# Performance work log

Measured on AMD Instinct MI355X. Metric: run time of the kernel, lower is better.

The kernel has to match this reference:

```python
import jax, jax.numpy as jnp
import numpy as np

B, T, DIM = 4, 2048, 512
HEADS, HD = 8, 64
RANK = 256
WIN = 256
EPS = 1e-6
ROPE_BASE = 10000.0


def _rope_tables(seq_len, head_dim):
    pos = jnp.arange(seq_len, dtype=jnp.float32)                      # [T]
    inv_freq = 1.0 / (ROPE_BASE ** (jnp.arange(0, head_dim, 2, dtype=jnp.float32) / head_dim))  # [HD/2]
    ang = pos[:, None] * inv_freq[None, :]                            # [T, HD/2]
    cos = jnp.concatenate([jnp.cos(ang), jnp.cos(ang)], axis=-1)      # [T, HD]
    sin = jnp.concatenate([jnp.sin(ang), jnp.sin(ang)], axis=-1)
    return cos, sin


def _rotate_half(x):
    x1, x2 = jnp.split(x, 2, axis=-1)
    return jnp.concatenate([-x2, x1], axis=-1)


def _apply_rope(q, k):
    # q, k: [B, H, T, HD]
    cos, sin = _rope_tables(q.shape[2], q.shape[3])
    cos = cos[None, None]; sin = sin[None, None]
    q = q * cos + _rotate_half(q) * sin
    k = k * cos + _rotate_half(k) * sin
    return q, k


def _rmsnorm(x, w):
    x32 = x.astype(jnp.float32)
    n = x32 * jax.lax.rsqrt(jnp.mean(x32 * x32, axis=-1, keepdims=True) + EPS)
    return n.astype(x.dtype) * w


def setup_inputs() -> dict:
    key = jax.random.key(0)
    ks = jax.random.split(key, 6)
    s = 0.02
    return {
        "x": jax.random.normal(ks[0], (B, T, DIM), dtype=jnp.float32),
        "Wq": jax.random.normal(ks[1], (DIM, DIM), dtype=jnp.float32) * s,
        "Wkv_down": jax.random.normal(ks[2], (RANK, DIM), dtype=jnp.float32) * s,
        "kv_norm_w": jnp.ones((RANK,), dtype=jnp.float32),
        "Wkv_up": jax.random.normal(ks[3], (2 * DIM, RANK), dtype=jnp.float32) * s,
        "Wout": jax.random.normal(ks[4], (DIM, DIM), dtype=jnp.float32) * s,
    }


def reference(x, Wq, Wkv_down, kv_norm_w, Wkv_up, Wout):
    # q projection -> [B, H, T, HD]
    q = jnp.einsum('btd,ed->bte', x, Wq).reshape(B, T, HEADS, HD).transpose(0, 2, 1, 3)
    # latent KV: down-proj -> RMSNorm -> up-proj
    c_kv = jnp.einsum('btd,rd->btr', x, Wkv_down)          # [B, T, RANK]
    c_kv = _rmsnorm(c_kv, kv_norm_w)
    kv = jnp.einsum('btr,er->bte', c_kv, Wkv_up)            # [B, T, 2*DIM]
    kv = kv.reshape(B, T, 2, HEADS, HD).transpose(2, 0, 3, 1, 4)
    k, v = kv[0], kv[1]                                     # [B, H, T, HD]
    q, k = _apply_rope(q, k)
    rows = jnp.arange(T)[:, None]
    cols = jnp.arange(T)[None, :]
    mask = jnp.abs(cols - rows) <= WIN                      # [T, T]
    scale = HD ** -0.5
    scores = jnp.einsum('bhtd,bhsd->bhts', q, k) * scale    # [B, H, T, T]
    scores = jnp.where(mask[None, None], scores, jnp.float32(-jnp.inf))
    attn = jax.nn.softmax(scores, axis=-1)
    out = jnp.einsum('bhts,bhsd->bhtd', attn, v)            # [B, H, T, HD]
    out = out.transpose(0, 2, 1, 3).reshape(B, T, DIM)
    return jnp.einsum('btd,ed->bte', out, Wout)
```

## Files before the change

kernel.cpp:

```cpp
#include <hip/hip_runtime.h>
#include <math.h>

#define BB 4
#define TT 2048
#define DIMM 512
#define HEADS 8
#define HDIM 64
#define RANKK 256
#define WINN 256

static constexpr int BT = BB * TT;
#define SC2 0.1803368801111244f

typedef short bf8_t __attribute__((ext_vector_type(8)));
typedef float f32x4 __attribute__((ext_vector_type(4)));

__device__ __forceinline__ unsigned short f2bf(float f) {
    unsigned u = __float_as_uint(f);
    u += 0x7fffu + ((u >> 16) & 1u);
    return (unsigned short)(u >> 16);
}
__device__ __forceinline__ unsigned f2bf2(float a, float b) {
    unsigned r;
    asm("v_cvt_pk_bf16_f32 %0, %1, %2" : "=v"(r) : "v"(a), "v"(b));
    return r;
}

typedef __attribute__((address_space(1))) void gvoid_t;
typedef __attribute__((address_space(3))) void lvoid_t;
__device__ __forceinline__ void gload16(const void* g, void* l) {
    __builtin_amdgcn_global_load_lds((gvoid_t*)g, (lvoid_t*)l, 16, 0, 0);
}
#define WAIT_VM0_BARRIER() do { \
    asm volatile("s_waitcnt vmcnt(0)" ::: "memory"); \
    __builtin_amdgcn_s_barrier(); \
    __builtin_amdgcn_sched_barrier(0); \
} while (0)

__device__ __forceinline__ void cvt4(const float* __restrict__ s,
                                     unsigned short* __restrict__ d, int i) {
    float4 v = *reinterpret_cast<const float4*>(s + i);
    uint2 st = make_uint2(f2bf2(v.x, v.y), f2bf2(v.z, v.w));
    *reinterpret_cast<uint2*>(d + i) = st;
}

__global__ __launch_bounds__(256) void prep_kernel(
    const float* __restrict__ x, const float* __restrict__ Wq,
    const float* __restrict__ Wkd, const float* __restrict__ Wku,
    const float* __restrict__ wn, const float* __restrict__ Wout,
    unsigned short* __restrict__ xb, unsigned short* __restrict__ wcomb,
    unsigned short* __restrict__ wkub, unsigned short* __restrict__ woutb,
    float* __restrict__ cosT, float* __restrict__ sinT) {
    int bid = blockIdx.x;
    if (bid < 4096) {
        cvt4(x, xb, (bid * 256 + threadIdx.x) * 4);
    } else if (bid < 4352) {
        cvt4(Wq, wcomb, ((bid - 4096) * 256 + threadIdx.x) * 4);
    } else if (bid < 4480) {
        cvt4(Wkd, wcomb + DIMM * DIMM, ((bid - 4352) * 256 + threadIdx.x) * 4);
    } else if (bid < 4736) {
        int i = ((bid - 4480) * 256 + threadIdx.x) * 4;
        float4 v = *reinterpret_cast<const float4*>(Wku + i);
        float4 s = *reinterpret_cast<const float4*>(wn + (i & 255));
        uint2 st = make_uint2(f2bf2(v.x * s.x, v.y * s.y), f2bf2(v.z * s.z, v.w * s.w));
        *reinterpret_cast<uint2*>(wkub + i) = st;
    } else if (bid < 4992) {
        cvt4(Wout, woutb, ((bid - 4736) * 256 + threadIdx.x) * 4);
    } else {
        int idx = (bid - 4992) * 256 + threadIdx.x;
        int t = idx >> 5, f = idx & 31;
        double freq = pow(10000.0, -(double)f / 32.0);
        double ang = (double)t * freq;
        cosT[idx] = (float)cos(ang);
        sinT[idx] = (float)sin(ang);
    }
}

template<int MODE, int BM>
__global__ __launch_bounds__(BM * 4) void gemm_bf(const unsigned short* __restrict__ A,
                                                  const unsigned short* __restrict__ W,
                                                  float* __restrict__ Cf,
                                                  unsigned short* __restrict__ O1,
                                                  unsigned short* __restrict__ O2,
                                                  const float* __restrict__ cosT,
                                                  const float* __restrict__ sinT,
                                                  float* __restrict__ ssum,
                                                  int K, int N) {
    __shared__ __align__(16) unsigned short As[2][BM * 64];
    __shared__ __align__(16) unsigned short Ws[2][128 * 64];
    const int tid = threadIdx.x;
    const int lane = tid & 63, w = tid >> 6;
    const int lr = lane & 15, hi = lane >> 4;
    const int m0 = blockIdx.x * BM, n0 = blockIdx.y * 128;
    const int wr = (w >> 1) * 32, wc = (w & 1) * 64;

    f32x4 acc[2][4];
#pragma unroll
    for (int i = 0; i < 2; ++i)
#pragma unroll
        for (int j = 0; j < 4; ++j) acc[i][j] = 0.0f;

    const int NT = K >> 6;
    auto stage = [&](int t, int b) {
        const int kt = t * 64;
#pragma unroll
        for (int c = tid; c < BM * 8; c += BM * 4) {
            int row = c >> 3, sc = ((c & 7) ^ (row & 7)) << 3;
            gload16(A + (size_t)(m0 + row) * K + kt + sc, &As[b][c * 8]);
        }
#pragma unroll
        for (int c = tid; c < 1024; c += BM * 4) {
            int row = c >> 3, sc = ((c & 7) ^ (row & 7)) << 3;
            gload16(W + (size_t)(n0 + row) * K + kt + sc, &Ws[b][c * 8]);
        }
    };

    stage(0, 0);
    WAIT_VM0_BARRIER();
    for (int t = 0; t < NT; ++t) {
        const int cur = t & 1;
        if (t + 1 < NT) stage(t + 1, cur ^ 1);
        bf8_t af[2][2], bw[4][2];
#pragma unroll
        for (int i = 0; i < 2; ++i) {
            int row = wr + i * 16 + lr;
#pragma unroll
            for (int kk = 0; kk < 2; ++kk)
                af[i][kk] = *reinterpret_cast<const bf8_t*>(
                    &As[cur][row * 64 + (((kk * 4 + hi) ^ (row & 7)) << 3)]);
        }
#pragma unroll
        for (int j = 0; j < 4; ++j) {
            int row = wc + j * 16 + lr;
#pragma unroll
            for (int kk = 0; kk < 2; ++kk)
                bw[j][kk] = *reinterpret_cast<const bf8_t*>(
                    &Ws[cur][row * 64 + (((kk * 4 + hi) ^ (row & 7)) << 3)]);
        }
#pragma unroll
        for (int kk = 0; kk < 2; ++kk)
#pragma unroll
            for (int i = 0; i < 2; ++i)
#pragma unroll
                for (int j = 0; j < 4; ++j)
                    acc[i][j] = __builtin_amdgcn_mfma_f32_16x16x32_bf16(af[i][kk], bw[j][kk], acc[i][j], 0, 0, 0);
        if (t + 1 < NT) WAIT_VM0_BARRIER();
    }

    if constexpr (MODE == 0) {
#pragma unroll
        for (int i = 0; i < 2; ++i)
#pragma unroll
            for (int j = 0; j < 4; ++j)
#pragma unroll
                for (int r = 0; r < 4; ++r)
                    Cf[(size_t)(m0 + wr + i * 16 + 4 * hi + r) * N + n0 + wc + j * 16 + lr] = acc[i][j][r];
    } else if (n0 < 512) {
        int h = (n0 + wc) >> 6;
#pragma unroll
        for (int i = 0; i < 2; ++i) {
            int tb = m0 + wr + i * 16 + 4 * hi;
            float4 rv4 = make_float4(1.f, 1.f, 1.f, 1.f);
            if constexpr (MODE == 2) {
                float4 sa = *reinterpret_cast<const float4*>(ssum + tb);
                float4 sb = *reinterpret_cast<const float4*>(ssum + 8192 + tb);
                float4 sc = *reinterpret_cast<const float4*>(ssum + 16384 + tb);
                float4 sd = *reinterpret_cast<const float4*>(ssum + 24576 + tb);
                rv4.x = rsqrtf((sa.x + sb.x + sc.x + sd.x) * (1.0f / RANKK) + 1e-6f);
                rv4.y = rsqrtf((sa.y + sb.y + sc.y + sd.y) * (1.0f / RANKK) + 1e-6f);
                rv4.z = rsqrtf((sa.z + sb.z + sc.z + sd.z) * (1.0f / RANKK) + 1e-6f);
                rv4.w = rsqrtf((sa.w + sb.w + sc.w + sd.w) * (1.0f / RANKK) + 1e-6f);
            }
#pragma unroll
            for (int j = 0; j < 2; ++j)
#pragma unroll
                for (int r = 0; r < 4; ++r) {
                    int t = tb + r;
                    int b = t >> 11, tt = t & 2047;
                    int ff = j * 16 + lr;
                    float rv = (&rv4.x)[r];
                    float x1 = acc[i][j][r] * rv, x2 = acc[i][j + 2][r] * rv;
                    float cc = cosT[tt * 32 + ff], ss = sinT[tt * 32 + ff];
                    unsigned u = f2bf2(x1 * cc - x2 * ss, x2 * cc + x1 * ss);
                    unsigned short* dp = O1 + ((size_t)((b * 8 + h) * 2048 + tt)) * 64;
                    dp[ff]      = (unsigned short)u;
                    dp[ff + 32] = (unsigned short)(u >> 16);
                }
        }
    } else if constexpr (MODE == 1) {
        int cb = n0 - 512 + wc;
        int part = ((n0 - 512) >> 7) * 2 + (w & 1);
#pragma unroll
        for (int i = 0; i < 2; ++i) {
            int tb = m0 + wr + i * 16 + 4 * hi;
#pragma unroll
            for (int r = 0; r < 4; ++r) {
                float ps = acc[i][0][r] * acc[i][0][r] + acc[i][1][r] * acc[i][1][r]
                         + acc[i][2][r] * acc[i][2][r] + acc[i][3][r] * acc[i][3][r];
                ps += __shfl_xor(ps, 1);
                ps += __shfl_xor(ps, 2);
                ps += __shfl_xor(ps, 4);
                ps += __shfl_xor(ps, 8);
                if (lr == 0) ssum[part * 8192 + tb + r] = ps;
            }
#pragma unroll
            for (int j = 0; j < 4; ++j) {
                unsigned a01 = f2bf2(acc[i][j][0], acc[i][j][1]);
                unsigned a23 = f2bf2(acc[i][j][2], acc[i][j][3]);
                unsigned short* dp = O2 + (size_t)tb * 256 + cb + j * 16 + lr;
                dp[0]   = (unsigned short)a01;
                dp[256] = (unsigned short)(a01 >> 16);
                dp[512] = (unsigned short)a23;
                dp[768] = (unsigned short)(a23 >> 16);
            }
        }
    } else {
        int cb = n0 + wc - 512;
        int h = cb >> 6;
#pragma unroll
        for (int i = 0; i < 2; ++i) {
            int tb = m0 + wr + i * 16 + 4 * hi;
            int b = tb >> 11, tt = tb & 2047;
            float4 sa = *reinterpret_cast<const float4*>(ssum + tb);
            float4 sb = *reinterpret_cast<const float4*>(ssum + 8192 + tb);
            float4 sc = *reinterpret_cast<const float4*>(ssum + 16384 + tb);
            float4 sd = *reinterpret_cast<const float4*>(ssum + 24576 + tb);
            float4 rv4;
            rv4.x = rsqrtf((sa.x + sb.x + sc.x + sd.x) * (1.0f / RANKK) + 1e-6f);
            rv4.y = rsqrtf((sa.y + sb.y + sc.y + sd.y) * (1.0f / RANKK) + 1e-6f);
            rv4.z = rsqrtf((sa.z + sb.z + sc.z + sd.z) * (1.0f / RANKK) + 1e-6f);
            rv4.w = rsqrtf((sa.w + sb.w + sc.w + sd.w) * (1.0f / RANKK) + 1e-6f);
#pragma unroll
            for (int j = 0; j < 4; ++j) {
                int hd = j * 16 + lr;
                uint2 st = make_uint2(f2bf2(acc[i][j][0] * rv4.x, acc[i][j][1] * rv4.y),
                                      f2bf2(acc[i][j][2] * rv4.z, acc[i][j][3] * rv4.w));
                *reinterpret_cast<uint2*>(O2 + (((size_t)(b * 8 + h) * 64 + hd) * 2048 + tt)) = st;
            }
        }
    }
}

__global__ __launch_bounds__(512) void attn_mfma(const unsigned short* __restrict__ qbf,
                                                 const unsigned short* __restrict__ kbf,
                                                 const unsigned short* __restrict__ vT,
                                                 unsigned short* __restrict__ aob) {
    __shared__ __align__(16) unsigned short Kl[2][64 * 64];
    __shared__ __align__(16) unsigned short Vl[2][64 * 64];
    __shared__ unsigned short Pl[128][72];
    const int tid = threadIdx.x;
    const int lane = tid & 63, w = tid >> 6;
    const int lr = lane & 15, hi = lane >> 4;

    const int fid = blockIdx.x;
    const int swz = (fid & 7) * 64 + (fid >> 3);
    const int t0 = (swz & 15) * 128;
    const int bh = swz >> 4;

    const unsigned short* qp = qbf + ((size_t)bh * TT + t0 + w * 16 + lr) * HDIM;
    bf8_t qa[2];
    qa[0] = *reinterpret_cast<const bf8_t*>(qp + hi * 8);
    qa[1] = *reinterpret_cast<const bf8_t*>(qp + 32 + hi * 8);

    f32x4 oc[4];
#pragma unroll
    for (int f = 0; f < 4; ++f) oc[f] = 0.0f;
    float lp[4] = {0.f, 0.f, 0.f, 0.f};

    const int smin = max(0, t0 - WINN);
    const int smax = min(TT, t0 + 128 + WINN);
    const int NT = (smax - smin) >> 6;

    const int st_row = tid >> 3;
    const int st_c = tid & 7;
    const int st_cs = (st_c ^ (st_row & 7)) << 3;

    auto stage = [&](int t, int b) {
        const int s0 = smin + t * 64;
        gload16(kbf + ((size_t)bh * TT + s0 + st_row) * HDIM + st_cs, &Kl[b][tid * 8]);
        gload16(vT + ((size_t)bh * 64 + st_row) * TT + s0 + st_cs, &Vl[b][tid * 8]);
    };

    stage(0, 0);
    WAIT_VM0_BARRIER();
    for (int t = 0; t < NT; ++t) {
        const int cur = t & 1;
        if (t + 1 < NT) stage(t + 1, cur ^ 1);
        const int s0 = smin + t * 64;

        f32x4 sacc[4];
#pragma unroll
        for (int f = 0; f < 4; ++f) sacc[f] = 0.0f;
        __builtin_amdgcn_s_setprio(1);
#pragma unroll
        for (int ks = 0; ks < 2; ++ks)
#pragma unroll
            for (int f = 0; f < 4; ++f) {
                int row = f * 16 + lr;
                bf8_t kb = *reinterpret_cast<const bf8_t*>(
                    &Kl[cur][row * 64 + (((ks * 4 + hi) ^ (row & 7)) << 3)]);
                sacc[f] = __builtin_amdgcn_mfma_f32_16x16x32_bf16(qa[ks], kb, sacc[f], 0, 0, 0);
            }
        __builtin_amdgcn_s_setprio(0);

        const int off_w = s0 - t0 - w * 16;
        const bool edge = (off_w + 63 > WINN) || (off_w - 15 < -WINN);
#pragma unroll
        for (int f = 0; f < 4; ++f) {
            float p[4];
#pragma unroll
            for (int r = 0; r < 4; ++r) {
                float v;
                if (edge) {
                    int d = off_w + f * 16 + lr - 4 * hi - r;
                    v = (d <= WINN && d >= -WINN) ? exp2f(sacc[f][r] * SC2) : 0.f;
                } else {
                    v = exp2f(sacc[f][r] * SC2);
                }
                p[r] = v;
                lp[r] += v;
            }
            unsigned a01 = f2bf2(p[0], p[1]);
            unsigned a23 = f2bf2(p[2], p[3]);
            unsigned short* bp = &Pl[w * 16 + 4 * hi][f * 16 + lr];
            bp[0]   = (unsigned short)a01;
            bp[72]  = (unsigned short)(a01 >> 16);
            bp[144] = (unsigned short)a23;
            bp[216] = (unsigned short)(a23 >> 16);
        }

        __builtin_amdgcn_s_setprio(1);
#pragma unroll
        for (int ks = 0; ks < 2; ++ks) {
            bf8_t pa = *reinterpret_cast<const bf8_t*>(&Pl[w * 16 + lr][ks * 32 + hi * 8]);
#pragma unroll
            for (int f = 0; f < 4; ++f) {
                int row = f * 16 + lr;
                bf8_t vb = *reinterpret_cast<const bf8_t*>(
                    &Vl[cur][row * 64 + (((ks * 4 + hi) ^ (row & 7)) << 3)]);
                oc[f] = __builtin_amdgcn_mfma_f32_16x16x32_bf16(pa, vb, oc[f], 0, 0, 0);
            }
        }
        __builtin_amdgcn_s_setprio(0);
        if (t + 1 < NT) WAIT_VM0_BARRIER();
    }

#pragma unroll
    for (int r = 0; r < 4; ++r) {
        lp[r] += __shfl_xor(lp[r], 1);
        lp[r] += __shfl_xor(lp[r], 2);
        lp[r] += __shfl_xor(lp[r], 4);
        lp[r] += __shfl_xor(lp[r], 8);
    }

    int b = bh >> 3, h = bh & 7;
#pragma unroll
    for (int r = 0; r < 4; ++r) {
        float inv = 1.0f / lp[r];
        int t = t0 + w * 16 + 4 * hi + r;
        unsigned short* op = aob + ((size_t)b * TT + t) * DIMM + h * HDIM;
        unsigned u0 = f2bf2(oc[0][r] * inv, oc[1][r] * inv);
        unsigned u1 = f2bf2(oc[2][r] * inv, oc[3][r] * inv);
        op[lr]      = (unsigned short)u0;
        op[16 + lr] = (unsigned short)(u0 >> 16);
        op[32 + lr] = (unsigned short)u1;
        op[48 + lr] = (unsigned short)(u1 >> 16);
    }
}

extern "C" void kernel_launch(void* const* d_in, const int* in_sizes, int n_in,
                              void* d_out, int out_size, void* d_ws, size_t ws_size,
                              hipStream_t stream) {
    const float* x     = (const float*)d_in[0];
    const float* Wq    = (const float*)d_in[1];
    const float* Wkd   = (const float*)d_in[2];
    const float* wnorm = (const float*)d_in[3];
    const float* Wku   = (const float*)d_in[4];
    const float* Wout  = (const float*)d_in[5];
    float* out = (float*)d_out;
    char* ws = (char*)d_ws;

    unsigned short* xb    = (unsigned short*)(ws + 0);
    unsigned short* qb    = (unsigned short*)(ws + 8388608);
    unsigned short* kb    = (unsigned short*)(ws + 16777216);
    unsigned short* vTb   = (unsigned short*)(ws + 25165824);
    unsigned short* ckvb0 = (unsigned short*)(ws + 33554432);
    unsigned short* aob   = (unsigned short*)(ws + 37748736);
    unsigned short* wcomb = (unsigned short*)(ws + 46137344);
    unsigned short* wkub  = (unsigned short*)(ws + 46923776);
    unsigned short* woutb = (unsigned short*)(ws + 47448064);
    float*          cosT  = (float*)(ws + 48005120);
    float*          sinT  = (float*)(ws + 48267264);
    float*          ssum  = (float*)(ws + 48529408);

    prep_kernel<<<5248, 256, 0, stream>>>(x, Wq, Wkd, Wku, wnorm, Wout,
                                          xb, wcomb, wkub, woutb, cosT, sinT);

    gemm_bf<1, 128><<<dim3(BT / 128, 6), 512, 0, stream>>>(xb, wcomb, nullptr, qb, ckvb0,
                                                           cosT, sinT, ssum, DIMM, 768);

    gemm_bf<2, 128><<<dim3(BT / 128, 8), 512, 0, stream>>>(ckvb0, wkub, nullptr, kb, vTb,
                                                           cosT, sinT, ssum, RANKK, 1024);

    attn_mfma<<<512, 512, 0, stream>>>(qb, kb, vTb, aob);

    gemm_bf<0, 64><<<dim3(BT / 64, 4), 256, 0, stream>>>(aob, woutb, out, nullptr, nullptr,
                                                         nullptr, nullptr, nullptr, DIMM, DIMM);
}
```

Measured before the change: 73.75 us.

## Give each attention wave two query tiles to reuse K/V fragments

The attention kernel now runs 4 waves per block instead of 8, and each wave handles 32 query rows as two 16-row tiles. Each K and V fragment read from LDS now feeds two MFMAs, halving LDS reads per MFMA and the number of waves synchronising at each barrier. The cost is more accumulator registers per wave and fewer waves per block to hide latency. Separately, the fused Q/KV-down GEMM launch moves from 128-row tiles with 512 threads to 64-row tiles with 256 threads, doubling its grid.

```diff
diff --git a/kernel.cpp b/kernel.cpp
--- a/kernel.cpp
+++ b/kernel.cpp
@@ -241,7 +241,7 @@
     }
 }
 
-__global__ __launch_bounds__(512) void attn_mfma(const unsigned short* __restrict__ qbf,
+__global__ __launch_bounds__(256) void attn_mfma(const unsigned short* __restrict__ qbf,
                                                  const unsigned short* __restrict__ kbf,
                                                  const unsigned short* __restrict__ vT,
                                                  unsigned short* __restrict__ aob) {
@@ -257,28 +257,34 @@
     const int t0 = (swz & 15) * 128;
     const int bh = swz >> 4;
 
-    const unsigned short* qp = qbf + ((size_t)bh * TT + t0 + w * 16 + lr) * HDIM;
-    bf8_t qa[2];
-    qa[0] = *reinterpret_cast<const bf8_t*>(qp + hi * 8);
-    qa[1] = *reinterpret_cast<const bf8_t*>(qp + 32 + hi * 8);
-
-    f32x4 oc[4];
-#pragma unroll
-    for (int f = 0; f < 4; ++f) oc[f] = 0.0f;
-    float lp[4] = {0.f, 0.f, 0.f, 0.f};
+    bf8_t qa[2][2];
+#pragma unroll
+    for (int qr = 0; qr < 2; ++qr) {
+        const unsigned short* qp = qbf + ((size_t)bh * TT + t0 + w * 32 + qr * 16 + lr) * HDIM;
+        qa[qr][0] = *reinterpret_cast<const bf8_t*>(qp + hi * 8);
+        qa[qr][1] = *reinterpret_cast<const bf8_t*>(qp + 32 + hi * 8);
+    }
+
+    f32x4 oc[2][4];
+#pragma unroll
+    for (int qr = 0; qr < 2; ++qr)
+#pragma unroll
+        for (int f = 0; f < 4; ++f) oc[qr][f] = 0.0f;
+    float lp[2][4] = {{0.f, 0.f, 0.f, 0.f}, {0.f, 0.f, 0.f, 0.f}};
 
     const int smin = max(0, t0 - WINN);
     const int smax = min(TT, t0 + 128 + WINN);
     const int NT = (smax - smin) >> 6;
 
-    const int st_row = tid >> 3;
-    const int st_c = tid & 7;
-    const int st_cs = (st_c ^ (st_row & 7)) << 3;
-
     auto stage = [&](int t, int b) {
         const int s0 = smin + t * 64;
-        gload16(kbf + ((size_t)bh * TT + s0 + st_row) * HDIM + st_cs, &Kl[b][tid * 8]);
-        gload16(vT + ((size_t)bh * 64 + st_row) * TT + s0 + st_cs, &Vl[b][tid * 8]);
+        int c0 = tid, c1 = tid + 256;
+        int row0 = c0 >> 3, sc0 = ((c0 & 7) ^ (row0 & 7)) << 3;
+        int row1 = c1 >> 3, sc1 = ((c1 & 7) ^ (row1 & 7)) << 3;
+        gload16(kbf + ((size_t)bh * TT + s0 + row0) * HDIM + sc0, &Kl[b][c0 * 8]);
+        gload16(kbf + ((size_t)bh * TT + s0 + row1) * HDIM + sc1, &Kl[b][c1 * 8]);
+        gload16(vT + ((size_t)bh * 64 + row0) * TT + s0 + sc0, &Vl[b][c0 * 8]);
+        gload16(vT + ((size_t)bh * 64 + row1) * TT + s0 + sc1, &Vl[b][c1 * 8]);
     };
 
     stage(0, 0);
@@ -288,9 +294,11 @@
         if (t + 1 < NT) stage(t + 1, cur ^ 1);
         const int s0 = smin + t * 64;
 
-        f32x4 sacc[4];
-#pragma unroll
-        for (int f = 0; f < 4; ++f) sacc[f] = 0.0f;
+        f32x4 sacc[2][4];
+#pragma unroll
+        for (int qr = 0; qr < 2; ++qr)
+#pragma unroll
+            for (int f = 0; f < 4; ++f) sacc[qr][f] = 0.0f;
         __builtin_amdgcn_s_setprio(1);
 #pragma unroll
         for (int ks = 0; ks < 2; ++ks)
@@ -299,46 +307,55 @@
                 int row = f * 16 + lr;
                 bf8_t kb = *reinterpret_cast<const bf8_t*>(
                     &Kl[cur][row * 64 + (((ks * 4 + hi) ^ (row & 7)) << 3)]);
-                sacc[f] = __builtin_amdgcn_mfma_f32_16x16x32_bf16(qa[ks], kb, sacc[f], 0, 0, 0);
+#pragma unroll
+                for (int qr = 0; qr < 2; ++qr)
+                    sacc[qr][f] = __builtin_amdgcn_mfma_f32_16x16x32_bf16(qa[qr][ks], kb, sacc[qr][f], 0, 0, 0);
             }
         __builtin_amdgcn_s_setprio(0);
 
-        const int off_w = s0 - t0 - w * 16;
-        const bool edge = (off_w + 63 > WINN) || (off_w - 15 < -WINN);
-#pragma unroll
-        for (int f = 0; f < 4; ++f) {
-            float p[4];
-#pragma unroll
-            for (int r = 0; r < 4; ++r) {
-                float v;
-                if (edge) {
-                    int d = off_w + f * 16 + lr - 4 * hi - r;
-                    v = (d <= WINN && d >= -WINN) ? exp2f(sacc[f][r] * SC2) : 0.f;
-                } else {
-                    v = exp2f(sacc[f][r] * SC2);
+        const int off_w = s0 - t0 - w * 32;
+        const bool edge = (off_w + 63 > WINN) || (off_w - 31 < -WINN);
+#pragma unroll
+        for (int qr = 0; qr < 2; ++qr)
+#pragma unroll
+            for (int f = 0; f < 4; ++f) {
+                float p[4];
+#pragma unroll
+                for (int r = 0; r < 4; ++r) {
+                    float v;
+                    if (edge) {
+                        int d = off_w + f * 16 + lr - qr * 16 - 4 * hi - r;
+                        v = (d <= WINN && d >= -WINN) ? exp2f(sacc[qr][f][r] * SC2) : 0.f;
+                    } else {
+                        v = exp2f(sacc[qr][f][r] * SC2);
+                    }
+                    p[r] = v;
+                    lp[qr][r] += v;
                 }
-                p[r] = v;
-                lp[r] += v;
-            }
-            unsigned a01 = f2bf2(p[0], p[1]);
-            unsigned a23 = f2bf2(p[2], p[3]);
-            unsigned short* bp = &Pl[w * 16 + 4 * hi][f * 16 + lr];
-            bp[0]   = (unsigned short)a01;
-            bp[72]  = (unsigned short)(a01 >> 16);
-            bp[144] = (unsigned short)a23;
-            bp[216] = (unsigned short)(a23 >> 16);
-        }
+                unsigned a01 = f2bf2(p[0], p[1]);
+                unsigned a23 = f2bf2(p[2], p[3]);
+                unsigned short* bp = &Pl[w * 32 + qr * 16 + 4 * hi][f * 16 + lr];
+                bp[0]   = (unsigned short)a01;
+                bp[72]  = (unsigned short)(a01 >> 16);
+                bp[144] = (unsigned short)a23;
+                bp[216] = (unsigned short)(a23 >> 16);
+            }
 
         __builtin_amdgcn_s_setprio(1);
 #pragma unroll
         for (int ks = 0; ks < 2; ++ks) {
-            bf8_t pa = *reinterpret_cast<const bf8_t*>(&Pl[w * 16 + lr][ks * 32 + hi * 8]);
+            bf8_t pa[2];
+#pragma unroll
+            for (int qr = 0; qr < 2; ++qr)
+                pa[qr] = *reinterpret_cast<const bf8_t*>(&Pl[w * 32 + qr * 16 + lr][ks * 32 + hi * 8]);
 #pragma unroll
             for (int f = 0; f < 4; ++f) {
                 int row = f * 16 + lr;
                 bf8_t vb = *reinterpret_cast<const bf8_t*>(
                     &Vl[cur][row * 64 + (((ks * 4 + hi) ^ (row & 7)) << 3)]);
-                oc[f] = __builtin_amdgcn_mfma_f32_16x16x32_bf16(pa, vb, oc[f], 0, 0, 0);
+#pragma unroll
+                for (int qr = 0; qr < 2; ++qr)
+                    oc[qr][f] = __builtin_amdgcn_mfma_f32_16x16x32_bf16(pa[qr], vb, oc[qr][f], 0, 0, 0);
             }
         }
         __builtin_amdgcn_s_setprio(0);
@@ -346,26 +363,30 @@
     }
 
 #pragma unroll
-    for (int r = 0; r < 4; ++r) {
-        lp[r] += __shfl_xor(lp[r], 1);
-        lp[r] += __shfl_xor(lp[r], 2);
-        lp[r] += __shfl_xor(lp[r], 4);
-        lp[r] += __shfl_xor(lp[r], 8);
-    }
+    for (int qr = 0; qr < 2; ++qr)
+#pragma unroll
+        for (int r = 0; r < 4; ++r) {
+            lp[qr][r] += __shfl_xor(lp[qr][r], 1);
+            lp[qr][r] += __shfl_xor(lp[qr][r], 2);
+            lp[qr][r] += __shfl_xor(lp[qr][r], 4);
+            lp[qr][r] += __shfl_xor(lp[qr][r], 8);
+        }
 
     int b = bh >> 3, h = bh & 7;
 #pragma unroll
-    for (int r = 0; r < 4; ++r) {
-        float inv = 1.0f / lp[r];
-        int t = t0 + w * 16 + 4 * hi + r;
-        unsigned short* op = aob + ((size_t)b * TT + t) * DIMM + h * HDIM;
-        unsigned u0 = f2bf2(oc[0][r] * inv, oc[1][r] * inv);
-        unsigned u1 = f2bf2(oc[2][r] * inv, oc[3][r] * inv);
-        op[lr]      = (unsigned short)u0;
-        op[16 + lr] = (unsigned short)(u0 >> 16);
-        op[32 + lr] = (unsigned short)u1;
-        op[48 + lr] = (unsigned short)(u1 >> 16);
-    }
+    for (int qr = 0; qr < 2; ++qr)
+#pragma unroll
+        for (int r = 0; r < 4; ++r) {
+            float inv = 1.0f / lp[qr][r];
+            int t = t0 + w * 32 + qr * 16 + 4 * hi + r;
+            unsigned short* op = aob + ((size_t)b * TT + t) * DIMM + h * HDIM;
+            unsigned u0 = f2bf2(oc[qr][0][r] * inv, oc[qr][1][r] * inv);
+            unsigned u1 = f2bf2(oc[qr][2][r] * inv, oc[qr][3][r] * inv);
+            op[lr]      = (unsigned short)u0;
+            op[16 + lr] = (unsigned short)(u0 >> 16);
+            op[32 + lr] = (unsigned short)u1;
+            op[48 + lr] = (unsigned short)(u1 >> 16);
+        }
 }
 
 extern "C" void kernel_launch(void* const* d_in, const int* in_sizes, int n_in,
@@ -396,13 +417,13 @@
     prep_kernel<<<5248, 256, 0, stream>>>(x, Wq, Wkd, Wku, wnorm, Wout,
                                           xb, wcomb, wkub, woutb, cosT, sinT);
 
-    gemm_bf<1, 128><<<dim3(BT / 128, 6), 512, 0, stream>>>(xb, wcomb, nullptr, qb, ckvb0,
-                                                           cosT, sinT, ssum, DIMM, 768);
+    gemm_bf<1, 64><<<dim3(BT / 64, 6), 256, 0, stream>>>(xb, wcomb, nullptr, qb, ckvb0,
+                                                         cosT, sinT, ssum, DIMM, 768);
 
     gemm_bf<2, 128><<<dim3(BT / 128, 8), 512, 0, stream>>>(ckvb0, wkub, nullptr, kb, vTb,
                                                            cosT, sinT, ssum, RANKK, 1024);
 
-    attn_mfma<<<512, 512, 0, stream>>>(qb, kb, vTb, aob);
+    attn_mfma<<<512, 256, 0, stream>>>(qb, kb, vTb, aob);
 
     gemm_bf<0, 64><<<dim3(BT / 64, 4), 256, 0, stream>>>(aob, woutb, out, nullptr, nullptr,
                                                          nullptr, nullptr, nullptr, DIMM, DIMM);
```

After: 81.19 us. +10.1%, slower.
